# Kernel optimization log

Hardware: AMD Instinct MI355X
Metric: run time of the kernel (lower is better)

Reference implementation:

```python
import jax, jax.numpy as jnp
import numpy as np

LATENT = 1024
ENC = 4096
B = 8192


def setup_inputs() -> dict:
    key = jax.random.key(0)
    k1, k2, k3, k4 = jax.random.split(key, 4)
    inp = jax.random.normal(k1, (B, LATENT), dtype=jnp.float32)
    enc = jax.random.normal(k2, (B, ENC), dtype=jnp.float32)
    # nn.Linear(ENC, LATENT): weight [LATENT, ENC], bias [LATENT]
    bound = 1.0 / np.sqrt(ENC)
    W = jax.random.uniform(k3, (LATENT, ENC), minval=-bound, maxval=bound, dtype=jnp.float32)
    b = jax.random.uniform(k4, (LATENT,), minval=-bound, maxval=bound, dtype=jnp.float32)
    return {"input": inp, "encoder_output": enc, "W": W, "b": b}


def reference(input, encoder_output, W, b):
    # vector = Linear(encoder_output)  -> [B, LATENT]
    v = jnp.einsum("be,de->bd", encoder_output, W) + b
    # Fused Householder-style reflection (math identical to bmm(vv^T, x)):
    # out = x - 2 * v * (v . x) / ||v||   (original divides by norm, not norm^2)
    dot = jnp.sum(v * input, axis=1, keepdims=True)          # [B, 1]
    norm = jnp.linalg.norm(v, axis=1, keepdims=True)         # [B, 1]
    output = input - 2.0 * v * dot / norm                    # [B, LATENT]
    log_det = jnp.zeros((input.shape[0], 1), dtype=input.dtype)
    return (output, log_det)
```

## Files before the change

### kernel.cpp

```cpp
#include <hip/hip_runtime.h>
#include <hip/hip_bf16.h>
#include <stdint.h>

#define M_DIM 8192
#define N_DIM 1024
#define K_DIM 4096

typedef __bf16 bf16x8 __attribute__((ext_vector_type(8)));
typedef float f32x4 __attribute__((ext_vector_type(4)));
typedef __hip_bfloat16 bf16_t;

__device__ __forceinline__ void gload_lds16(const void* g, void* l) {
  __builtin_amdgcn_global_load_lds(
      (const __attribute__((address_space(1))) void*)g,
      (__attribute__((address_space(3))) void*)l, 16, 0, 0);
}

__device__ __forceinline__ float b2f(unsigned short u) {
  union { unsigned i; float f; } x;
  x.i = ((unsigned)u) << 16;
  return x.f;
}

__global__ __launch_bounds__(256) void pack_both(const float* __restrict__ enc,
                                                 const float* __restrict__ W,
                                                 int4* __restrict__ pA,
                                                 int4* __restrict__ pB) {
  const unsigned gtid = blockIdx.x * 256 + threadIdx.x;
  const float* src;
  int4* dst;
  unsigned t;
  if (gtid < 4194304u) { src = enc; dst = pA; t = gtid; }
  else                 { src = W;   dst = pB; t = gtid - 4194304u; }
  const unsigned cp = t & 7;
  const unsigned tmp = t >> 3;
  const unsigned r = tmp & 255;
  const unsigned tmp2 = tmp >> 8;
  const unsigned kt = tmp2 & 63;
  const unsigned rt = tmp2 >> 6;
  const unsigned srow = (rt << 8) + r;
  const unsigned k0 = (kt << 6) + ((cp ^ (r & 7)) << 3);
  const float4* s = (const float4*)(src + (size_t)srow * 4096 + k0);
  float4 a = s[0], b = s[1];
  union { bf16_t h[8]; int4 v; } u;
  u.h[0] = __float2bfloat16(a.x); u.h[1] = __float2bfloat16(a.y);
  u.h[2] = __float2bfloat16(a.z); u.h[3] = __float2bfloat16(a.w);
  u.h[4] = __float2bfloat16(b.x); u.h[5] = __float2bfloat16(b.y);
  u.h[6] = __float2bfloat16(b.z); u.h[7] = __float2bfloat16(b.w);
  dst[t] = u.v;
}

__device__ __forceinline__ void stage_half(const char* g, char* smem, int ldsoff, int tid) {
  gload_lds16(g + tid * 16, smem + ldsoff + tid * 16);
  gload_lds16(g + 8192 + tid * 16, smem + ldsoff + 8192 + tid * 16);
}

__global__ __launch_bounds__(512, 2) void gemm8(
    const char* __restrict__ pA, const char* __restrict__ pB,
    bf16_t* __restrict__ V0, bf16_t* __restrict__ V1p, int NT) {
  extern __shared__ char smem[];
  const int tid = threadIdx.x;
  const int lane = tid & 63, wave = tid >> 6;
  const int wm = wave >> 2, wn = wave & 3;
  const int lrow = lane & 15, lkc = lane >> 4;

  const int cpx = (int)gridDim.x >> 3;
  const int swz = ((int)blockIdx.x & 7) * cpx + ((int)blockIdx.x >> 3);
  const int split = swz >> 7;
  const int rem = swz & 127;
  const int mt = rem >> 2, nt = rem & 3;

  const char* Abase = pA + ((size_t)mt * 64 + (size_t)split * NT) * 32768;
  const char* Bbase = pB + ((size_t)nt * 64 + (size_t)split * NT) * 32768;
  bf16_t* V = split ? V1p : V0;

  int colw[2];
  colw[0] = ((lkc) ^ (lrow & 7)) << 4;
  colw[1] = ((4 + lkc) ^ (lrow & 7)) << 4;
  int aRow[4], bRow[2];
  #pragma unroll
  for (int f = 0; f < 4; ++f) aRow[f] = (wm * 64 + f * 16 + lrow) * 128;
  #pragma unroll
  for (int f2 = 0; f2 < 2; ++f2) bRow[f2] = 32768 + (wn * 32 + f2 * 16 + lrow) * 128;

  f32x4 acc[2][4][2][2];
  #pragma unroll
  for (int a0 = 0; a0 < 2; ++a0)
    #pragma unroll
    for (int a1 = 0; a1 < 4; ++a1)
      #pragma unroll
      for (int a2 = 0; a2 < 2; ++a2)
        #pragma unroll
        for (int a3 = 0; a3 < 2; ++a3)
          acc[a0][a1][a2][a3] = (f32x4){0.f, 0.f, 0.f, 0.f};

  const int ktm = NT - 1;

  stage_half(Abase,         smem, 0, tid);
  stage_half(Bbase,         smem, 32768, tid);
  stage_half(Bbase + 16384, smem, 49152, tid);
  stage_half(Abase + 16384, smem, 16384, tid);
  stage_half(Abase + 32768, smem, 65536, tid);
  asm volatile("s_waitcnt vmcnt(4)" ::: "memory");
  __builtin_amdgcn_sched_barrier(0);
  __builtin_amdgcn_s_barrier();

  bf16x8 aE[4][2], aO[4][2], b0[2][2], b1[2][2];
  #pragma unroll
  for (int f = 0; f < 4; ++f)
    #pragma unroll
    for (int s = 0; s < 2; ++s)
      aE[f][s] = *(const bf16x8*)(smem + aRow[f] + colw[s]);
  #pragma unroll
  for (int f2 = 0; f2 < 2; ++f2)
    #pragma unroll
    for (int s = 0; s < 2; ++s)
      b0[f2][s] = *(const bf16x8*)(smem + bRow[f2] + colw[s]);

  for (int g = 0; g < NT; ++g) {
    const int bb = g & 1, nbf = bb ^ 1;
    char* ab = smem + bb * 65536;
    char* nb = smem + nbf * 65536;
    const char* A1t = Abase + (size_t)((g + 1) & ktm) * 32768;
    const char* B1t = Bbase + (size_t)((g + 1) & ktm) * 32768;
    const char* A2t = Abase + (size_t)((g + 2) & ktm) * 32768;

    stage_half(B1t, smem, nbf * 65536 + 32768, tid);
    stage_half(B1t + 16384, smem, nbf * 65536 + 49152, tid);
    __builtin_amdgcn_s_setprio(1);
    #pragma unroll
    for (int f = 0; f < 4; ++f)
      #pragma unroll
      for (int f2 = 0; f2 < 2; ++f2)
        #pragma unroll
        for (int s = 0; s < 2; ++s)
          acc[0][f][0][f2] = __builtin_amdgcn_mfma_f32_16x16x32_bf16(
              aE[f][s], b0[f2][s], acc[0][f][0][f2], 0, 0, 0);
    __builtin_amdgcn_s_setprio(0);
    __builtin_amdgcn_sched_barrier(0);
    #pragma unroll
    for (int f2 = 0; f2 < 2; ++f2)
      #pragma unroll
      for (int s = 0; s < 2; ++s)
        b1[f2][s] = *(const bf16x8*)(ab + bRow[f2] + 16384 + colw[s]);
    asm volatile("s_waitcnt vmcnt(6)" ::: "memory");
    __builtin_amdgcn_sched_barrier(0);
    __builtin_amdgcn_s_barrier();

    stage_half(A1t + 16384, smem, nbf * 65536 + 16384, tid);
    __builtin_amdgcn_s_setprio(1);
    #pragma unroll
    for (int f = 0; f < 4; ++f)
      #pragma unroll
      for (int f2 = 0; f2 < 2; ++f2)
        #pragma unroll
        for (int s = 0; s < 2; ++s)
          acc[0][f][1][f2] = __builtin_amdgcn_mfma_f32_16x16x32_bf16(
              aE[f][s], b1[f2][s], acc[0][f][1][f2], 0, 0, 0);
    __builtin_amdgcn_s_setprio(0);
    __builtin_amdgcn_sched_barrier(0);
    #pragma unroll
    for (int f = 0; f < 4; ++f)
      #pragma unroll
      for (int s = 0; s < 2; ++s)
        aO[f][s] = *(const bf16x8*)(ab + aRow[f] + 16384 + colw[s]);
    __builtin_amdgcn_sched_barrier(0);
    __builtin_amdgcn_s_barrier();

    stage_half(A2t, smem, bb * 65536, tid);
    __builtin_amdgcn_s_setprio(1);
    #pragma unroll
    for (int f = 0; f < 4; ++f)
      #pragma unroll
      for (int f2 = 0; f2 < 2; ++f2)
        #pragma unroll
        for (int s = 0; s < 2; ++s)
          acc[1][f][1][f2] = __builtin_amdgcn_mfma_f32_16x16x32_bf16(
              aO[f][s], b1[f2][s], acc[1][f][1][f2], 0, 0, 0);
    __builtin_amdgcn_s_setprio(0);
    __builtin_amdgcn_sched_barrier(0);
    asm volatile("s_waitcnt vmcnt(8)" ::: "memory");
    #pragma unroll
    for (int f = 0; f < 4; ++f)
      #pragma unroll
      for (int s = 0; s < 2; ++s)
        aE[f][s] = *(const bf16x8*)(nb + aRow[f] + colw[s]);
    __builtin_amdgcn_sched_barrier(0);
    __builtin_amdgcn_s_barrier();

    __builtin_amdgcn_s_setprio(1);
    #pragma unroll
    for (int f = 0; f < 4; ++f)
      #pragma unroll
      for (int f2 = 0; f2 < 2; ++f2)
        #pragma unroll
        for (int s = 0; s < 2; ++s)
          acc[1][f][0][f2] = __builtin_amdgcn_mfma_f32_16x16x32_bf16(
              aO[f][s], b0[f2][s], acc[1][f][0][f2], 0, 0, 0);
    __builtin_amdgcn_s_setprio(0);
    __builtin_amdgcn_sched_barrier(0);
    asm volatile("s_waitcnt vmcnt(4)" ::: "memory");
    #pragma unroll
    for (int f2 = 0; f2 < 2; ++f2)
      #pragma unroll
      for (int s = 0; s < 2; ++s)
        b0[f2][s] = *(const bf16x8*)(nb + bRow[f2] + colw[s]);
    __builtin_amdgcn_sched_barrier(0);
    __builtin_amdgcn_s_barrier();
  }

  const int lq = lane >> 4;
  #pragma unroll
  for (int qm = 0; qm < 2; ++qm)
    #pragma unroll
    for (int f = 0; f < 4; ++f) {
      const int rowg = mt * 256 + qm * 128 + wm * 64 + f * 16 + lq * 4;
      #pragma unroll
      for (int reg = 0; reg < 4; ++reg) {
        bf16_t* Vr = V + (size_t)(rowg + reg) * N_DIM + nt * 256 + wn * 32 + lrow;
        #pragma unroll
        for (int qn = 0; qn < 2; ++qn)
          #pragma unroll
          for (int f2 = 0; f2 < 2; ++f2)
            Vr[qn * 128 + f2 * 16] = __float2bfloat16(acc[qm][f][qn][f2][reg]);
      }
    }
}

__global__ __launch_bounds__(256) void householder_ep(
    const float* __restrict__ x, const float* __restrict__ bias,
    const unsigned short* __restrict__ V0b, const unsigned short* __restrict__ V1b,
    float* __restrict__ out, float* __restrict__ logdet) {
  const int row = blockIdx.x;
  const int t = threadIdx.x;
  const float4* xr = (const float4*)(x + (size_t)row * N_DIM);
  const float4* br = (const float4*)bias;

  ushort4 u0 = ((const ushort4*)(V0b + (size_t)row * N_DIM))[t];
  float4 v;
  v.x = b2f(u0.x); v.y = b2f(u0.y); v.z = b2f(u0.z); v.w = b2f(u0.w);
  if (V1b) {
    ushort4 u1 = ((const ushort4*)(V1b + (size_t)row * N_DIM))[t];
    v.x += b2f(u1.x); v.y += b2f(u1.y); v.z += b2f(u1.z); v.w += b2f(u1.w);
  }
  float4 bb = br[t];
  v.x += bb.x; v.y += bb.y; v.z += bb.z; v.w += bb.w;
  float4 xx = xr[t];

  float dot = v.x * xx.x + v.y * xx.y + v.z * xx.z + v.w * xx.w;
  float nsq = v.x * v.x + v.y * v.y + v.z * v.z + v.w * v.w;

  #pragma unroll
  for (int off = 32; off > 0; off >>= 1) {
    dot += __shfl_down(dot, off);
    nsq += __shfl_down(nsq, off);
  }
  __shared__ float sd[4], sn[4];
  if ((t & 63) == 0) { sd[t >> 6] = dot; sn[t >> 6] = nsq; }
  __syncthreads();
  dot = sd[0] + sd[1] + sd[2] + sd[3];
  nsq = sn[0] + sn[1] + sn[2] + sn[3];

  const float f = 2.0f * dot / sqrtf(nsq);
  float4 o;
  o.x = xx.x - f * v.x;
  o.y = xx.y - f * v.y;
  o.z = xx.z - f * v.z;
  o.w = xx.w - f * v.w;
  ((float4*)(out + (size_t)row * N_DIM))[t] = o;
  if (t == 0) logdet[row] = 0.0f;
}

extern "C" void kernel_launch(void* const* d_in, const int* in_sizes, int n_in,
                              void* d_out, int out_size, void* d_ws, size_t ws_size,
                              hipStream_t stream) {
  const float* x   = (const float*)d_in[0];
  const float* enc = (const float*)d_in[1];
  const float* W   = (const float*)d_in[2];
  const float* b   = (const float*)d_in[3];

  float* out    = (float*)d_out;
  float* logdet = out + (size_t)M_DIM * N_DIM;

  char*   packA = (char*)d_ws;
  char*   packB = packA + (size_t)64 * 1024 * 1024;
  bf16_t* V0b   = (bf16_t*)(packB + (size_t)8 * 1024 * 1024);
  bf16_t* V1b   = V0b + (size_t)M_DIM * N_DIM;

  const size_t need2 = (size_t)104 * 1024 * 1024;
  const int nsplit = (ws_size >= need2) ? 2 : 1;

  pack_both<<<18432, 256, 0, stream>>>(enc, W, (int4*)packA, (int4*)packB);

  hipFuncSetAttribute((const void*)gemm8, hipFuncAttributeMaxDynamicSharedMemorySize, 131072);
  gemm8<<<dim3(128 * nsplit), 512, 131072, stream>>>(
      packA, packB, V0b, nsplit == 2 ? V1b : nullptr, 64 / nsplit);

  householder_ep<<<M_DIM, 256, 0, stream>>>(
      x, b, (const unsigned short*)V0b,
      nsplit == 2 ? (const unsigned short*)V1b : nullptr, out, logdet);
}
```

Before: 116.2 us.

## Fuse pack, GEMM and Householder epilogue into one cooperative persistent kernel

Result: slower. 331.4 us (+185.1%).

```diff
diff --git a/kernel.cpp b/kernel.cpp
--- a/kernel.cpp
+++ b/kernel.cpp
@@ -1,6 +1,9 @@
 #include <hip/hip_runtime.h>
 #include <hip/hip_bf16.h>
+#include <hip/hip_cooperative_groups.h>
 #include <stdint.h>
+
+namespace cg = cooperative_groups;
 
 #define M_DIM 8192
 #define N_DIM 1024
@@ -22,16 +25,8 @@
   return x.f;
 }
 
-__global__ __launch_bounds__(256) void pack_both(const float* __restrict__ enc,
-                                                 const float* __restrict__ W,
-                                                 int4* __restrict__ pA,
-                                                 int4* __restrict__ pB) {
-  const unsigned gtid = blockIdx.x * 256 + threadIdx.x;
-  const float* src;
-  int4* dst;
-  unsigned t;
-  if (gtid < 4194304u) { src = enc; dst = pA; t = gtid; }
-  else                 { src = W;   dst = pB; t = gtid - 4194304u; }
+__device__ __forceinline__ void pack_one(const float* __restrict__ src,
+                                         int4* __restrict__ dst, unsigned t) {
   const unsigned cp = t & 7;
   const unsigned tmp = t >> 3;
   const unsigned r = tmp & 255;
@@ -55,6 +50,255 @@
   gload_lds16(g + 8192 + tid * 16, smem + ldsoff + 8192 + tid * 16);
 }
 
+__device__ void gemm_body(const char* __restrict__ pA, const char* __restrict__ pB,
+                          bf16_t* __restrict__ V0, bf16_t* __restrict__ V1p,
+                          char* smem, int tid, int bid, int nblocks) {
+  const int lane = tid & 63, wave = tid >> 6;
+  const int wm = wave >> 2, wn = wave & 3;
+  const int lrow = lane & 15, lkc = lane >> 4;
+  const int NT = 32, ktm = 31;
+
+  const int cpx = nblocks >> 3;
+  const int swz = (bid & 7) * cpx + (bid >> 3);
+  const int split = swz >> 7;
+  const int rem = swz & 127;
+  const int mt = rem >> 2, nt = rem & 3;
+
+  const char* Abase = pA + ((size_t)mt * 64 + (size_t)split * NT) * 32768;
+  const char* Bbase = pB + ((size_t)nt * 64 + (size_t)split * NT) * 32768;
+  bf16_t* V = split ? V1p : V0;
+
+  int colw[2];
+  colw[0] = ((lkc) ^ (lrow & 7)) << 4;
+  colw[1] = ((4 + lkc) ^ (lrow & 7)) << 4;
+  int aRow[4], bRow[2];
+  #pragma unroll
+  for (int f = 0; f < 4; ++f) aRow[f] = (wm * 64 + f * 16 + lrow) * 128;
+  #pragma unroll
+  for (int f2 = 0; f2 < 2; ++f2) bRow[f2] = 32768 + (wn * 32 + f2 * 16 + lrow) * 128;
+
+  f32x4 acc[2][4][2][2];
+  #pragma unroll
+  for (int a0 = 0; a0 < 2; ++a0)
+    #pragma unroll
+    for (int a1 = 0; a1 < 4; ++a1)
+      #pragma unroll
+      for (int a2 = 0; a2 < 2; ++a2)
+        #pragma unroll
+        for (int a3 = 0; a3 < 2; ++a3)
+          acc[a0][a1][a2][a3] = (f32x4){0.f, 0.f, 0.f, 0.f};
+
+  stage_half(Abase,         smem, 0, tid);
+  stage_half(Bbase,         smem, 32768, tid);
+  stage_half(Bbase + 16384, smem, 49152, tid);
+  stage_half(Abase + 16384, smem, 16384, tid);
+  stage_half(Abase + 32768, smem, 65536, tid);
+  asm volatile("s_waitcnt vmcnt(4)" ::: "memory");
+  __builtin_amdgcn_sched_barrier(0);
+  __builtin_amdgcn_s_barrier();
+
+  bf16x8 aE[4][2], aO[4][2], b0[2][2], b1[2][2];
+  #pragma unroll
+  for (int f = 0; f < 4; ++f)
+    #pragma unroll
+    for (int s = 0; s < 2; ++s)
+      aE[f][s] = *(const bf16x8*)(smem + aRow[f] + colw[s]);
+  #pragma unroll
+  for (int f2 = 0; f2 < 2; ++f2)
+    #pragma unroll
+    for (int s = 0; s < 2; ++s)
+      b0[f2][s] = *(const bf16x8*)(smem + bRow[f2] + colw[s]);
+
+  for (int g = 0; g < NT; ++g) {
+    const int bb = g & 1, nbf = bb ^ 1;
+    char* ab = smem + bb * 65536;
+    char* nb = smem + nbf * 65536;
+    const char* A1t = Abase + (size_t)((g + 1) & ktm) * 32768;
+    const char* B1t = Bbase + (size_t)((g + 1) & ktm) * 32768;
+    const char* A2t = Abase + (size_t)((g + 2) & ktm) * 32768;
+
+    stage_half(B1t, smem, nbf * 65536 + 32768, tid);
+    stage_half(B1t + 16384, smem, nbf * 65536 + 49152, tid);
+    __builtin_amdgcn_s_setprio(1);
+    #pragma unroll
+    for (int f = 0; f < 4; ++f)
+      #pragma unroll
+      for (int f2 = 0; f2 < 2; ++f2)
+        #pragma unroll
+        for (int s = 0; s < 2; ++s)
+          acc[0][f][0][f2] = __builtin_amdgcn_mfma_f32_16x16x32_bf16(
+              aE[f][s], b0[f2][s], acc[0][f][0][f2], 0, 0, 0);
+    __builtin_amdgcn_s_setprio(0);
+    __builtin_amdgcn_sched_barrier(0);
+    #pragma unroll
+    for (int f2 = 0; f2 < 2; ++f2)
+      #pragma unroll
+      for (int s = 0; s < 2; ++s)
+        b1[f2][s] = *(const bf16x8*)(ab + bRow[f2] + 16384 + colw[s]);
+    asm volatile("s_waitcnt vmcnt(6)" ::: "memory");
+    __builtin_amdgcn_sched_barrier(0);
+    __builtin_amdgcn_s_barrier();
+
+    stage_half(A1t + 16384, smem, nbf * 65536 + 16384, tid);
+    __builtin_amdgcn_s_setprio(1);
+    #pragma unroll
+    for (int f = 0; f < 4; ++f)
+      #pragma unroll
+      for (int f2 = 0; f2 < 2; ++f2)
+        #pragma unroll
+        for (int s = 0; s < 2; ++s)
+          acc[0][f][1][f2] = __builtin_amdgcn_mfma_f32_16x16x32_bf16(
+              aE[f][s], b1[f2][s], acc[0][f][1][f2], 0, 0, 0);
+    __builtin_amdgcn_s_setprio(0);
+    __builtin_amdgcn_sched_barrier(0);
+    #pragma unroll
+    for (int f = 0; f < 4; ++f)
+      #pragma unroll
+      for (int s = 0; s < 2; ++s)
+        aO[f][s] = *(const bf16x8*)(ab + aRow[f] + 16384 + colw[s]);
+    __builtin_amdgcn_sched_barrier(0);
+    __builtin_amdgcn_s_barrier();
+
+    stage_half(A2t, smem, bb * 65536, tid);
+    __builtin_amdgcn_s_setprio(1);
+    #pragma unroll
+    for (int f = 0; f < 4; ++f)
+      #pragma unroll
+      for (int f2 = 0; f2 < 2; ++f2)
+        #pragma unroll
+        for (int s = 0; s < 2; ++s)
+          acc[1][f][1][f2] = __builtin_amdgcn_mfma_f32_16x16x32_bf16(
+              aO[f][s], b1[f2][s], acc[1][f][1][f2], 0, 0, 0);
+    __builtin_amdgcn_s_setprio(0);
+    __builtin_amdgcn_sched_barrier(0);
+    asm volatile("s_waitcnt vmcnt(8)" ::: "memory");
+    #pragma unroll
+    for (int f = 0; f < 4; ++f)
+      #pragma unroll
+      for (int s = 0; s < 2; ++s)
+        aE[f][s] = *(const bf16x8*)(nb + aRow[f] + colw[s]);
+    __builtin_amdgcn_sched_barrier(0);
+    __builtin_amdgcn_s_barrier();
+
+    __builtin_amdgcn_s_setprio(1);
+    #pragma unroll
+    for (int f = 0; f < 4; ++f)
+      #pragma unroll
+      for (int f2 = 0; f2 < 2; ++f2)
+        #pragma unroll
+        for (int s = 0; s < 2; ++s)
+          acc[1][f][0][f2] = __builtin_amdgcn_mfma_f32_16x16x32_bf16(
+              aO[f][s], b0[f2][s], acc[1][f][0][f2], 0, 0, 0);
+    __builtin_amdgcn_s_setprio(0);
+    __builtin_amdgcn_sched_barrier(0);
+    asm volatile("s_waitcnt vmcnt(4)" ::: "memory");
+    #pragma unroll
+    for (int f2 = 0; f2 < 2; ++f2)
+      #pragma unroll
+      for (int s = 0; s < 2; ++s)
+        b0[f2][s] = *(const bf16x8*)(nb + bRow[f2] + colw[s]);
+    __builtin_amdgcn_sched_barrier(0);
+    __builtin_amdgcn_s_barrier();
+  }
+
+  const int lq = lane >> 4;
+  #pragma unroll
+  for (int qm = 0; qm < 2; ++qm)
+    #pragma unroll
+    for (int f = 0; f < 4; ++f) {
+      const int rowg = mt * 256 + qm * 128 + wm * 64 + f * 16 + lq * 4;
+      #pragma unroll
+      for (int reg = 0; reg < 4; ++reg) {
+        bf16_t* Vr = V + (size_t)(rowg + reg) * N_DIM + nt * 256 + wn * 32 + lrow;
+        #pragma unroll
+        for (int qn = 0; qn < 2; ++qn)
+          #pragma unroll
+          for (int f2 = 0; f2 < 2; ++f2)
+            Vr[qn * 128 + f2 * 16] = __float2bfloat16(acc[qm][f][qn][f2][reg]);
+      }
+    }
+}
+
+__global__ __launch_bounds__(512, 2) void fused(
+    const float* __restrict__ enc, const float* __restrict__ W,
+    const float* __restrict__ x, const float* __restrict__ bias,
+    char* __restrict__ packA, char* __restrict__ packB,
+    bf16_t* __restrict__ V0, bf16_t* __restrict__ V1,
+    float* __restrict__ out, float* __restrict__ logdet) {
+  extern __shared__ char smem[];
+  cg::grid_group grid = cg::this_grid();
+  const int tid = threadIdx.x;
+  const int bid = blockIdx.x;
+
+  {
+    const unsigned base = (unsigned)bid * 512u + (unsigned)tid;
+    #pragma unroll 4
+    for (int it = 0; it < 36; ++it) {
+      unsigned gt = (unsigned)it * 131072u + base;
+      if (gt < 4194304u) pack_one(enc, (int4*)packA, gt);
+      else               pack_one(W,   (int4*)packB, gt - 4194304u);
+    }
+  }
+  __threadfence();
+  grid.sync();
+
+  gemm_body(packA, packB, V0, V1, smem, tid, bid, (int)gridDim.x);
+  __threadfence();
+  grid.sync();
+
+  {
+    const int half = tid >> 8;
+    const int t2 = tid & 255;
+    float* sred = (float*)smem;
+    for (int it = 0; it < 16; ++it) {
+      const int row = bid * 32 + it * 2 + half;
+      ushort4 u0 = ((const ushort4*)((const unsigned short*)V0 + (size_t)row * N_DIM))[t2];
+      ushort4 u1 = ((const ushort4*)((const unsigned short*)V1 + (size_t)row * N_DIM))[t2];
+      float4 bb = ((const float4*)bias)[t2];
+      float4 v;
+      v.x = b2f(u0.x) + b2f(u1.x) + bb.x;
+      v.y = b2f(u0.y) + b2f(u1.y) + bb.y;
+      v.z = b2f(u0.z) + b2f(u1.z) + bb.z;
+      v.w = b2f(u0.w) + b2f(u1.w) + bb.w;
+      float4 xx = ((const float4*)(x + (size_t)row * N_DIM))[t2];
+
+      float dot = v.x * xx.x + v.y * xx.y + v.z * xx.z + v.w * xx.w;
+      float nsq = v.x * v.x + v.y * v.y + v.z * v.z + v.w * v.w;
+      #pragma unroll
+      for (int off = 32; off > 0; off >>= 1) {
+        dot += __shfl_down(dot, off);
+        nsq += __shfl_down(nsq, off);
+      }
+      if ((t2 & 63) == 0) {
+        sred[half * 8 + (t2 >> 6)] = dot;
+        sred[half * 8 + 4 + (t2 >> 6)] = nsq;
+      }
+      __syncthreads();
+      dot = sred[half * 8] + sred[half * 8 + 1] + sred[half * 8 + 2] + sred[half * 8 + 3];
+      nsq = sred[half * 8 + 4] + sred[half * 8 + 5] + sred[half * 8 + 6] + sred[half * 8 + 7];
+      const float f = 2.0f * dot / sqrtf(nsq);
+      float4 o;
+      o.x = xx.x - f * v.x;
+      o.y = xx.y - f * v.y;
+      o.z = xx.z - f * v.z;
+      o.w = xx.w - f * v.w;
+      ((float4*)(out + (size_t)row * N_DIM))[t2] = o;
+      if (t2 == 0 && half == 0) logdet[row] = 0.0f;
+      if (t2 == 0 && half == 1) logdet[row] = 0.0f;
+      __syncthreads();
+    }
+  }
+}
+
+__global__ __launch_bounds__(256) void pack_both(const float* __restrict__ enc,
+                                                 const float* __restrict__ W,
+                                                 int4* __restrict__ pA,
+                                                 int4* __restrict__ pB) {
+  const unsigned gtid = blockIdx.x * 256 + threadIdx.x;
+  if (gtid < 4194304u) pack_one(enc, pA, gtid);
+  else                 pack_one(W,   pB, gtid - 4194304u);
+}
+
 __global__ __launch_bounds__(512, 2) void gemm8(
     const char* __restrict__ pA, const char* __restrict__ pB,
     bf16_t* __restrict__ V0, bf16_t* __restrict__ V1p, int NT) {
@@ -63,16 +307,15 @@
   const int lane = tid & 63, wave = tid >> 6;
   const int wm = wave >> 2, wn = wave & 3;
   const int lrow = lane & 15, lkc = lane >> 4;
-
   const int cpx = (int)gridDim.x >> 3;
   const int swz = ((int)blockIdx.x & 7) * cpx + ((int)blockIdx.x >> 3);
-  const int split = swz >> 7;
   const int rem = swz & 127;
   const int mt = rem >> 2, nt = rem & 3;
-
-  const char* Abase = pA + ((size_t)mt * 64 + (size_t)split * NT) * 32768;
-  const char* Bbase = pB + ((size_t)nt * 64 + (size_t)split * NT) * 32768;
-  bf16_t* V = split ? V1p : V0;
+  const int ktm = NT - 1;
+  const char* Abase = pA + (size_t)mt * 64 * 32768;
+  const char* Bbase = pB + (size_t)nt * 64 * 32768;
+  bf16_t* V = V0;
+  (void)V1p;
 
   int colw[2];
   colw[0] = ((lkc) ^ (lrow & 7)) << 4;
@@ -93,8 +336,6 @@
         #pragma unroll
         for (int a3 = 0; a3 < 2; ++a3)
           acc[a0][a1][a2][a3] = (f32x4){0.f, 0.f, 0.f, 0.f};
-
-  const int ktm = NT - 1;
 
   stage_half(Abase,         smem, 0, tid);
   stage_half(Bbase,         smem, 32768, tid);
@@ -102,7 +343,6 @@
   stage_half(Abase + 16384, smem, 16384, tid);
   stage_half(Abase + 32768, smem, 65536, tid);
   asm volatile("s_waitcnt vmcnt(4)" ::: "memory");
-  __builtin_amdgcn_sched_barrier(0);
   __builtin_amdgcn_s_barrier();
 
   bf16x8 aE[4][2], aO[4][2], b0[2][2], b1[2][2];
@@ -127,7 +367,6 @@
 
     stage_half(B1t, smem, nbf * 65536 + 32768, tid);
     stage_half(B1t + 16384, smem, nbf * 65536 + 49152, tid);
-    __builtin_amdgcn_s_setprio(1);
     #pragma unroll
     for (int f = 0; f < 4; ++f)
       #pragma unroll
@@ -136,19 +375,15 @@
         for (int s = 0; s < 2; ++s)
           acc[0][f][0][f2] = __builtin_amdgcn_mfma_f32_16x16x32_bf16(
               aE[f][s], b0[f2][s], acc[0][f][0][f2], 0, 0, 0);
-    __builtin_amdgcn_s_setprio(0);
-    __builtin_amdgcn_sched_barrier(0);
     #pragma unroll
     for (int f2 = 0; f2 < 2; ++f2)
       #pragma unroll
       for (int s = 0; s < 2; ++s)
         b1[f2][s] = *(const bf16x8*)(ab + bRow[f2] + 16384 + colw[s]);
     asm volatile("s_waitcnt vmcnt(6)" ::: "memory");
-    __builtin_amdgcn_sched_barrier(0);
     __builtin_amdgcn_s_barrier();
 
     stage_half(A1t + 16384, smem, nbf * 65536 + 16384, tid);
-    __builtin_amdgcn_s_setprio(1);
     #pragma unroll
     for (int f = 0; f < 4; ++f)
       #pragma unroll
@@ -157,18 +392,14 @@
         for (int s = 0; s < 2; ++s)
           acc[0][f][1][f2] = __builtin_amdgcn_mfma_f32_16x16x32_bf16(
               aE[f][s], b1[f2][s], acc[0][f][1][f2], 0, 0, 0);
-    __builtin_amdgcn_s_setprio(0);
-    __builtin_amdgcn_sched_barrier(0);
     #pragma unroll
     for (int f = 0; f < 4; ++f)
       #pragma unroll
       for (int s = 0; s < 2; ++s)
         aO[f][s] = *(const bf16x8*)(ab + aRow[f] + 16384 + colw[s]);
-    __builtin_amdgcn_sched_barrier(0);
     __builtin_amdgcn_s_barrier();
 
     stage_half(A2t, smem, bb * 65536, tid);
-    __builtin_amdgcn_s_setprio(1);
     #pragma unroll
     for (int f = 0; f < 4; ++f)
       #pragma unroll
@@ -177,18 +408,14 @@
         for (int s = 0; s < 2; ++s)
           acc[1][f][1][f2] = __builtin_amdgcn_mfma_f32_16x16x32_bf16(
               aO[f][s], b1[f2][s], acc[1][f][1][f2], 0, 0, 0);
-    __builtin_amdgcn_s_setprio(0);
-    __builtin_amdgcn_sched_barrier(0);
     asm volatile("s_waitcnt vmcnt(8)" ::: "memory");
     #pragma unroll
     for (int f = 0; f < 4; ++f)
       #pragma unroll
       for (int s = 0; s < 2; ++s)
         aE[f][s] = *(const bf16x8*)(nb + aRow[f] + colw[s]);
-    __builtin_amdgcn_sched_barrier(0);
-    __builtin_amdgcn_s_barrier();
-
-    __builtin_amdgcn_s_setprio(1);
+    __builtin_amdgcn_s_barrier();
+
     #pragma unroll
     for (int f = 0; f < 4; ++f)
       #pragma unroll
@@ -197,15 +424,12 @@
         for (int s = 0; s < 2; ++s)
           acc[1][f][0][f2] = __builtin_amdgcn_mfma_f32_16x16x32_bf16(
               aO[f][s], b0[f2][s], acc[1][f][0][f2], 0, 0, 0);
-    __builtin_amdgcn_s_setprio(0);
-    __builtin_amdgcn_sched_barrier(0);
     asm volatile("s_waitcnt vmcnt(4)" ::: "memory");
     #pragma unroll
     for (int f2 = 0; f2 < 2; ++f2)
       #pragma unroll
       for (int s = 0; s < 2; ++s)
         b0[f2][s] = *(const bf16x8*)(nb + bRow[f2] + colw[s]);
-    __builtin_amdgcn_sched_barrier(0);
     __builtin_amdgcn_s_barrier();
   }
 
@@ -233,9 +457,6 @@
     float* __restrict__ out, float* __restrict__ logdet) {
   const int row = blockIdx.x;
   const int t = threadIdx.x;
-  const float4* xr = (const float4*)(x + (size_t)row * N_DIM);
-  const float4* br = (const float4*)bias;
-
   ushort4 u0 = ((const ushort4*)(V0b + (size_t)row * N_DIM))[t];
   float4 v;
   v.x = b2f(u0.x); v.y = b2f(u0.y); v.z = b2f(u0.z); v.w = b2f(u0.w);
@@ -243,13 +464,12 @@
     ushort4 u1 = ((const ushort4*)(V1b + (size_t)row * N_DIM))[t];
     v.x += b2f(u1.x); v.y += b2f(u1.y); v.z += b2f(u1.z); v.w += b2f(u1.w);
   }
-  float4 bb = br[t];
+  float4 bb = ((const float4*)bias)[t];
   v.x += bb.x; v.y += bb.y; v.z += bb.z; v.w += bb.w;
-  float4 xx = xr[t];
+  float4 xx = ((const float4*)(x + (size_t)row * N_DIM))[t];
 
   float dot = v.x * xx.x + v.y * xx.y + v.z * xx.z + v.w * xx.w;
   float nsq = v.x * v.x + v.y * v.y + v.z * v.z + v.w * v.w;
-
   #pragma unroll
   for (int off = 32; off > 0; off >>= 1) {
     dot += __shfl_down(dot, off);
@@ -260,7 +480,6 @@
   __syncthreads();
   dot = sd[0] + sd[1] + sd[2] + sd[3];
   nsq = sn[0] + sn[1] + sn[2] + sn[3];
-
   const float f = 2.0f * dot / sqrtf(nsq);
   float4 o;
   o.x = xx.x - f * v.x;
@@ -288,15 +507,19 @@
   bf16_t* V1b   = V0b + (size_t)M_DIM * N_DIM;
 
   const size_t need2 = (size_t)104 * 1024 * 1024;
-  const int nsplit = (ws_size >= need2) ? 2 : 1;
-
-  pack_both<<<18432, 256, 0, stream>>>(enc, W, (int4*)packA, (int4*)packB);
-
-  hipFuncSetAttribute((const void*)gemm8, hipFuncAttributeMaxDynamicSharedMemorySize, 131072);
-  gemm8<<<dim3(128 * nsplit), 512, 131072, stream>>>(
-      packA, packB, V0b, nsplit == 2 ? V1b : nullptr, 64 / nsplit);
-
-  householder_ep<<<M_DIM, 256, 0, stream>>>(
-      x, b, (const unsigned short*)V0b,
-      nsplit == 2 ? (const unsigned short*)V1b : nullptr, out, logdet);
-}
+
+  if (ws_size >= need2) {
+    hipFuncSetAttribute((const void*)fused, hipFuncAttributeMaxDynamicSharedMemorySize, 131072);
+    void* kargs[] = {(void*)&enc, (void*)&W, (void*)&x, (void*)&b,
+                     (void*)&packA, (void*)&packB, (void*)&V0b, (void*)&V1b,
+                     (void*)&out, (void*)&logdet};
+    hipLaunchCooperativeKernel((const void*)fused, dim3(256), dim3(512),
+                               kargs, 131072, stream);
+  } else {
+    pack_both<<<18432, 256, 0, stream>>>(enc, W, (int4*)packA, (int4*)packB);
+    hipFuncSetAttribute((const void*)gemm8, hipFuncAttributeMaxDynamicSharedMemorySize, 131072);
+    gemm8<<<dim3(128), 512, 131072, stream>>>(packA, packB, V0b, nullptr, 64);
+    householder_ep<<<M_DIM, 256, 0, stream>>>(
+        x, b, (const unsigned short*)V0b, nullptr, out, logdet);
+  }
+}
```
